# Kernel tuning notes

Hardware: AMD Instinct MI355X
Metric: run time of the kernel (lower is better)

The kernel has to match this reference:

```python
import jax, jax.numpy as jnp
import numpy as np

N_NODES = 50000
N_EDGES = 800000
NFEAT, NHID, NCLASS = 512, 128, 16


def _with_self_loops(edge_idx, n):
    loop = jnp.arange(n, dtype=edge_idx.dtype)
    src = jnp.concatenate([edge_idx[0], loop])  # [E+N]
    dst = jnp.concatenate([edge_idx[1], loop])
    return src, dst


def gcn_conv(x, src, dst, W, b, n):
    # GCNConv with add aggregation, self-loops, symmetric normalization.
    h = x @ W  # [N, out]
    ones = jnp.ones(src.shape[0], dtype=h.dtype)
    deg = jax.ops.segment_sum(ones, dst, num_segments=n)  # in-degree incl. self-loops
    dinv = jnp.where(deg > 0, jax.lax.rsqrt(deg), 0.0)
    norm = dinv[src] * dinv[dst]  # [E+N]
    msg = h[src] * norm[:, None]  # gather + scale
    out = jax.ops.segment_sum(msg, dst, num_segments=n)  # scatter-add
    return out + b


def setup_inputs() -> dict:
    key = jax.random.key(0)
    ks = jax.random.split(key, 8)
    x = jax.random.normal(ks[0], (N_NODES, NFEAT), dtype=jnp.float32)
    edge_idx = jax.random.randint(ks[1], (2, N_EDGES), 0, N_NODES, dtype=jnp.int64)
    s1 = 1.0 / np.sqrt(NFEAT)
    s2 = 1.0 / np.sqrt(NHID)
    W1 = jax.random.uniform(ks[2], (NFEAT, NHID), jnp.float32, -s1, s1)
    b1 = jnp.zeros((NHID,), jnp.float32)
    W2 = jax.random.uniform(ks[3], (NHID, NHID), jnp.float32, -s2, s2)
    b2 = jnp.zeros((NHID,), jnp.float32)
    Wc = jax.random.uniform(ks[4], (NHID, NCLASS), jnp.float32, -s2, s2)
    bc = jax.random.uniform(ks[5], (NCLASS,), jnp.float32, -s2, s2)
    return {"x": x, "edge_idx": edge_idx, "W1": W1, "b1": b1, "W2": W2, "b2": b2, "Wc": Wc, "bc": bc}


def reference(x, edge_idx, W1, b1, W2, b2, Wc, bc):
    n = x.shape[0]
    src, dst = _with_self_loops(edge_idx, n)
    h = gcn_conv(x, src, dst, W1, b1, n)
    h = jax.nn.relu(h)  # dropout is identity in eval mode
    h = gcn_conv(h, src, dst, W2, b2, n)
    h = jax.nn.relu(h)
    logits = h @ Wc + bc
    return jax.nn.log_softmax(logits, axis=1)
```

## Files before the change

### kernel.cpp

```cpp
#include <hip/hip_runtime.h>
#include <math.h>

#define NFEAT 512
#define NHID  128
#define NCLASS 16
#define SCAN_BS 512
#define AGG_BLOCKS 2048

typedef __attribute__((ext_vector_type(8))) short short8;
typedef __attribute__((ext_vector_type(4))) float f32x4;

static __device__ __forceinline__ ushort f2b(float f) {
    union { float f; uint u; } v; v.f = f;
    uint r = v.u + 0x7FFFu + ((v.u >> 16) & 1u);
    return (ushort)(r >> 16);
}
static __device__ __forceinline__ float b2f_lo(uint bits) {
    union { uint u; float f; } v; v.u = bits << 16; return v.f;
}
static __device__ __forceinline__ float b2f_hi(uint bits) {
    union { uint u; float f; } v; v.u = bits & 0xffff0000u; return v.f;
}
static __device__ __forceinline__ float b2f(uint bits) {
    union { uint u; float f; } v; v.u = bits << 16; return v.f;
}


__global__ void k_init_deg(int* __restrict__ deg, int n) {
    int i = blockIdx.x * blockDim.x + threadIdx.x;
    if (i < n) deg[i] = 1;
}

__global__ void k_count(const int* __restrict__ dst, int e, int* __restrict__ deg) {
    int i = blockIdx.x * blockDim.x + threadIdx.x;
    if (i < e) atomicAdd(&deg[dst[i]], 1);
}

__global__ void k_dinv(const int* __restrict__ deg, float* __restrict__ dinv,
                       int* __restrict__ gcnt, int* __restrict__ cursor, int n) {
    int i = blockIdx.x * blockDim.x + threadIdx.x;
    if (i < n) {
        dinv[i] = rsqrtf((float)deg[i]);
        gcnt[i] = (deg[i] + 7) >> 3;
        cursor[i] = 0;
    }
}

__global__ void k_scan1(const int* __restrict__ in, int* __restrict__ offs,
                        int* __restrict__ bsum, int n) {
    __shared__ int s[SCAN_BS];
    int t = threadIdx.x;
    int i = blockIdx.x * SCAN_BS + t;
    int v = (i < n) ? in[i] : 0;
    s[t] = v;
    for (int off = 1; off < SCAN_BS; off <<= 1) {
        __syncthreads();
        int x = (t >= off) ? s[t - off] : 0;
        __syncthreads();
        s[t] += x;
    }
    __syncthreads();
    if (i < n) offs[i] = s[t] - v;
    if (t == SCAN_BS - 1) bsum[blockIdx.x] = s[t];
}

__global__ void k_scan2(int* __restrict__ bsum, int* __restrict__ offs, int nb, int n) {
    if (threadIdx.x == 0 && blockIdx.x == 0) {
        int run = 0;
        for (int b = 0; b < nb; b++) { int x = bsum[b]; bsum[b] = run; run += x; }
        offs[n] = run;
    }
}

__global__ void k_scan3(int* __restrict__ offs, const int* __restrict__ bsum, int n) {
    int i = blockIdx.x * SCAN_BS + threadIdx.x;
    if (i < n) offs[i] += bsum[blockIdx.x];
}

__global__ void k_fill_edges(const int* __restrict__ src, const int* __restrict__ dst, int e,
                             const int* __restrict__ goffs, int* __restrict__ cursor,
                             ushort* __restrict__ colp) {
    int i = blockIdx.x * blockDim.x + threadIdx.x;
    if (i < e) {
        int d = dst[i];
        int p = atomicAdd(&cursor[d], 1);
        colp[(size_t)goffs[d] * 8 + p] = (ushort)src[i];
    }
}

__global__ void k_fill_tail(const int* __restrict__ goffs, const int* __restrict__ deg,
                            ushort* __restrict__ colp, int* __restrict__ gnode,
                            ushort* __restrict__ hs, int n) {
    int i = blockIdx.x * blockDim.x + threadIdx.x;
    if (i < 128) {
        int s = i >> 5, f = i & 31;
        hs[((size_t)s * (n + 1) + n) * 32 + f] = 0;
    }
    if (i < n) {
        int g0 = goffs[i], g1 = goffs[i + 1];
        size_t base = (size_t)g0 * 8;
        int d = deg[i];
        int slots = (g1 - g0) * 8;
        colp[base + d - 1] = (ushort)i;
        for (int p = d; p < slots; p++) colp[base + p] = (ushort)n;
        for (int g = g0; g < g1; g++) gnode[g] = i;
        if (i == 0) {
            int G = goffs[n];
            gnode[G] = -1;
            for (int k = 0; k < 16; k++) colp[(size_t)G * 8 + k] = (ushort)n;
        }
    }
}


__global__ void k_tcast(const float* __restrict__ W, ushort* __restrict__ WT, int K) {
    int idx = blockIdx.x * 256 + threadIdx.x;
    if (idx < K * 128) {
        int k = idx >> 7, c = idx & 127;
        WT[(size_t)c * K + k] = f2b(W[idx]);
    }
}


template<int A_F32>
__global__ __launch_bounds__(256) void k_gemm(const void* __restrict__ Aptr,
                                              const ushort* __restrict__ WT,
                                              const float* __restrict__ rowscale,
                                              ushort* __restrict__ Hs, int M, int K) {
    __shared__ ushort As[128][40];
    __shared__ ushort Bs[128][40];

    const int tid = threadIdx.x;
    const int wid = tid >> 6, lane = tid & 63;
    const int wr = wid >> 1, wc = wid & 1;
    const int lr = lane & 15, lk = (lane >> 4) * 8;
    const int rowbase = blockIdx.x * 128;

    f32x4 acc[4][4];
#pragma unroll
    for (int i = 0; i < 4; i++)
#pragma unroll
        for (int j = 0; j < 4; j++) acc[i][j] = (f32x4)0.f;

    const int sr = tid >> 1;
    const int sh = (tid & 1) * 16;

    for (int k0 = 0; k0 < K; k0 += 32) {
        {
            int gr = rowbase + sr;
            ushort tmp[16];
            if (A_F32) {
                const float* A = (const float*)Aptr;
                if (gr < M) {
                    const float* p = A + (size_t)gr * K + k0 + sh;
#pragma unroll
                    for (int q = 0; q < 4; q++) {
                        float4 v = *(const float4*)(p + q * 4);
                        tmp[q * 4 + 0] = f2b(v.x); tmp[q * 4 + 1] = f2b(v.y);
                        tmp[q * 4 + 2] = f2b(v.z); tmp[q * 4 + 3] = f2b(v.w);
                    }
                } else {
#pragma unroll
                    for (int q = 0; q < 16; q++) tmp[q] = 0;
                }
            } else {
                const ushort* A = (const ushort*)Aptr;
                if (gr < M) {
                    const ushort* p = A + (size_t)gr * K + k0 + sh;
                    *(short8*)&tmp[0] = *(const short8*)(p);
                    *(short8*)&tmp[8] = *(const short8*)(p + 8);
                } else {
#pragma unroll
                    for (int q = 0; q < 16; q++) tmp[q] = 0;
                }
            }
            *(short8*)&As[sr][sh]     = *(short8*)&tmp[0];
            *(short8*)&As[sr][sh + 8] = *(short8*)&tmp[8];
        }
        {
#pragma unroll
            for (int t = 0; t < 2; t++) {
                int c = tid + t * 256;
                int row = c >> 2, q = c & 3;
                short8 v = *(const short8*)(WT + (size_t)row * K + k0 + q * 8);
                *(short8*)&Bs[row][q * 8] = v;
            }
        }
        __syncthreads();

        short8 af[4], bfv[4];
#pragma unroll
        for (int i = 0; i < 4; i++) af[i] = *(const short8*)&As[wr * 64 + i * 16 + lr][lk];
#pragma unroll
        for (int j = 0; j < 4; j++) bfv[j] = *(const short8*)&Bs[wc * 64 + j * 16 + lr][lk];
#pragma unroll
        for (int i = 0; i < 4; i++)
#pragma unroll
            for (int j = 0; j < 4; j++)
                acc[i][j] = __builtin_amdgcn_mfma_f32_16x16x32_bf16(af[i], bfv[j], acc[i][j], 0, 0, 0);
        __syncthreads();
    }

#pragma unroll
    for (int i = 0; i < 4; i++) {
#pragma unroll
        for (int r = 0; r < 4; r++) {
            int row = rowbase + wr * 64 + i * 16 + (lane >> 4) * 4 + r;
            if (row < M) {
                float sc = rowscale[row];
#pragma unroll
                for (int j = 0; j < 4; j++) {
                    int slice = wc * 2 + (j >> 1);
                    int f = (j & 1) * 16 + lr;
                    Hs[((size_t)slice * (M + 1) + row) * 32 + f] = f2b(acc[i][j][r] * sc);
                }
            }
        }
    }
}


__global__ __launch_bounds__(256) void k_aggs(const ushort* __restrict__ hs,
                                              const int* __restrict__ goffs,
                                              const ushort* __restrict__ colp,
                                              const int* __restrict__ gnode,
                                              const float* __restrict__ dinv,
                                              const float* __restrict__ bias,
                                              ushort* __restrict__ outp, int n) {
    const int b = blockIdx.x;
    const int s = (b & 7) >> 1;
    const int wid = threadIdx.x >> 6, lane = threadIdx.x & 63;
    const int e8 = lane >> 3, q = lane & 7;

    const int G = goffs[n];
    const int nranks = gridDim.x;
    const int rank = ((b >> 3) * 2 + (b & 1)) * 4 + wid;
    const int run = (G + nranks - 1) / nranks;
    int gs = rank * run;
    if (gs >= G) return;
    int ge = gs + run; if (ge > G) ge = G;
    if (gs > 0) {
        int pv = gnode[gs - 1];
        while (gs < ge && gnode[gs] == pv) gs++;
        if (gs >= ge) return;
    }

    const ushort* hsl = hs + (size_t)s * (n + 1) * 32;
    const float4 bv = *(const float4*)(bias + s * 32 + q * 4);

    int g = gs;
    const ushort* cp = colp + (size_t)g * 8 + e8;
    const int* gp = gnode + g;
    int v = gp[0];
    uint sc0 = cp[0];
    uint sc1 = cp[8];
    float a0 = 0.f, a1 = 0.f, a2 = 0.f, a3 = 0.f;

    while (true) {
        uint sc2 = cp[16];
        int v_n = gp[1];
        uint2 pk = *(const uint2*)(hsl + (size_t)sc0 * 32 + q * 4);
        a0 += b2f_lo(pk.x); a1 += b2f_hi(pk.x);
        a2 += b2f_lo(pk.y); a3 += b2f_hi(pk.y);

        if (v_n != v) {
            float dv = dinv[v];
            float r0 = a0, r1 = a1, r2 = a2, r3 = a3;
#pragma unroll
            for (int off = 8; off <= 32; off <<= 1) {
                r0 += __shfl_xor(r0, off); r1 += __shfl_xor(r1, off);
                r2 += __shfl_xor(r2, off); r3 += __shfl_xor(r3, off);
            }
            r0 = fmaxf(fmaf(r0, dv, bv.x), 0.f);
            r1 = fmaxf(fmaf(r1, dv, bv.y), 0.f);
            r2 = fmaxf(fmaf(r2, dv, bv.z), 0.f);
            r3 = fmaxf(fmaf(r3, dv, bv.w), 0.f);
            if (lane < 8) {
                uint2 u;
                u.x = (uint)f2b(r0) | ((uint)f2b(r1) << 16);
                u.y = (uint)f2b(r2) | ((uint)f2b(r3) << 16);
                *(uint2*)(outp + (size_t)v * 128 + s * 32 + q * 4) = u;
            }
            if (g + 1 >= ge) break;
            v = v_n;
            a0 = a1 = a2 = a3 = 0.f;
        }
        g++; gp++; cp += 8;
        sc0 = sc1; sc1 = sc2;
    }
}


__global__ __launch_bounds__(256) void k_classify(const ushort* __restrict__ h,
                                                  const float* __restrict__ Wc,
                                                  const float* __restrict__ bc,
                                                  float* __restrict__ out, int n) {
    __shared__ float Ws[128 * 16];
    int tid = threadIdx.x;
#pragma unroll
    for (int t = 0; t < 8; t++) Ws[tid + 256 * t] = Wc[tid + 256 * t];
    __syncthreads();

    int wid = tid >> 6, lane = tid & 63;
    int v = blockIdx.x * 4 + wid;
    if (v >= n) return;

    int j = lane & 15, c = lane >> 4;
    const ushort* hv = h + (size_t)v * 128 + c * 32;
    float acc = 0.f;
#pragma unroll
    for (int t = 0; t < 16; t++) {
        uint pk = *(const uint*)(hv + t * 2);
        acc = fmaf(b2f_lo(pk), Ws[(c * 32 + t * 2 + 0) * 16 + j], acc);
        acc = fmaf(b2f_hi(pk), Ws[(c * 32 + t * 2 + 1) * 16 + j], acc);
    }
    acc += __shfl_xor(acc, 16);
    acc += __shfl_xor(acc, 32);
    acc += bc[j];

    float m = acc;
#pragma unroll
    for (int o = 8; o >= 1; o >>= 1) m = fmaxf(m, __shfl_xor(m, o));
    float sum = expf(acc - m);
#pragma unroll
    for (int o = 8; o >= 1; o >>= 1) sum += __shfl_xor(sum, o);
    if (lane < 16) out[(size_t)v * 16 + j] = acc - m - logf(sum);
}


extern "C" void kernel_launch(void* const* d_in, const int* in_sizes, int n_in,
                              void* d_out, int out_size, void* d_ws, size_t ws_size,
                              hipStream_t stream) {
    const float* x  = (const float*)d_in[0];
    const int* eidx = (const int*)d_in[1];
    const float* W1 = (const float*)d_in[2];
    const float* b1 = (const float*)d_in[3];
    const float* W2 = (const float*)d_in[4];
    const float* b2 = (const float*)d_in[5];
    const float* Wc = (const float*)d_in[6];
    const float* bc = (const float*)d_in[7];
    float* out = (float*)d_out;

    const int N = in_sizes[0] / NFEAT;
    const int E = in_sizes[1] / 2;
    const int* src = eidx;
    const int* dst = eidx + E;

    char* p = (char*)d_ws;
    auto alloc = [&](size_t bytes) { char* r = p; p += (bytes + 255) & ~(size_t)255; return r; };
    int*    deg    = (int*)   alloc((size_t)N * 4);
    float*  dinv   = (float*) alloc((size_t)N * 4);
    int*    gcnt   = (int*)   alloc((size_t)N * 4);
    int*    goffs  = (int*)   alloc((size_t)(N + 1) * 4);
    int*    cursor = (int*)   alloc((size_t)N * 4);
    ushort* colp   = (ushort*)alloc(((size_t)E + 8ull * N + 32) * 2);
    int*    gnode  = (int*)   alloc(((size_t)E / 8 + N + 2) * 4);
    int*    bsum   = (int*)   alloc((size_t)256 * 4);
    ushort* W1T    = (ushort*)alloc((size_t)128 * NFEAT * 2);
    ushort* W2T    = (ushort*)alloc((size_t)128 * NHID * 2);
    ushort* hs     = (ushort*)alloc((size_t)(N + 1) * NHID * 2);
    ushort* g1     = (ushort*)alloc((size_t)N * NHID * 2);
    ushort* g2     = (ushort*)alloc((size_t)N * NHID * 2);

    const int nb = (N + SCAN_BS - 1) / SCAN_BS;

    k_init_deg<<<(N + 255) / 256, 256, 0, stream>>>(deg, N);
    k_count<<<(E + 255) / 256, 256, 0, stream>>>(dst, E, deg);
    k_dinv<<<(N + 255) / 256, 256, 0, stream>>>(deg, dinv, gcnt, cursor, N);
    k_scan1<<<nb, SCAN_BS, 0, stream>>>(gcnt, goffs, bsum, N);
    k_scan2<<<1, 64, 0, stream>>>(bsum, goffs, nb, N);
    k_scan3<<<nb, SCAN_BS, 0, stream>>>(goffs, bsum, N);
    k_fill_edges<<<(E + 255) / 256, 256, 0, stream>>>(src, dst, E, goffs, cursor, colp);
    k_fill_tail<<<(N + 255) / 256, 256, 0, stream>>>(goffs, deg, colp, gnode, hs, N);

    k_tcast<<<(NFEAT * 128 + 255) / 256, 256, 0, stream>>>(W1, W1T, NFEAT);
    k_tcast<<<(NHID * 128 + 255) / 256, 256, 0, stream>>>(W2, W2T, NHID);

    const int gblocks = (N + 127) / 128;
    k_gemm<1><<<gblocks, 256, 0, stream>>>(x, W1T, dinv, hs, N, NFEAT);
    k_aggs<<<AGG_BLOCKS, 256, 0, stream>>>(hs, goffs, colp, gnode, dinv, b1, g1, N);
    k_gemm<0><<<gblocks, 256, 0, stream>>>(g1, W2T, dinv, hs, N, NHID);
    k_aggs<<<AGG_BLOCKS, 256, 0, stream>>>(hs, goffs, colp, gnode, dinv, b2, g2, N);
    k_classify<<<(N + 3) / 4, 256, 0, stream>>>(g2, Wc, bc, out, N);
}
```

Baseline: 276.0 us.

## Pack node-end metadata into 32-bit column words and deepen aggregation prefetch

```diff
diff --git a/kernel.cpp b/kernel.cpp
--- a/kernel.cpp
+++ b/kernel.cpp
@@ -20,9 +20,6 @@
 }
 static __device__ __forceinline__ float b2f_hi(uint bits) {
     union { uint u; float f; } v; v.u = bits & 0xffff0000u; return v.f;
-}
-static __device__ __forceinline__ float b2f(uint bits) {
-    union { uint u; float f; } v; v.u = bits << 16; return v.f;
 }
 
 
@@ -79,18 +76,17 @@
 
 __global__ void k_fill_edges(const int* __restrict__ src, const int* __restrict__ dst, int e,
                              const int* __restrict__ goffs, int* __restrict__ cursor,
-                             ushort* __restrict__ colp) {
+                             uint* __restrict__ colp32) {
     int i = blockIdx.x * blockDim.x + threadIdx.x;
     if (i < e) {
         int d = dst[i];
         int p = atomicAdd(&cursor[d], 1);
-        colp[(size_t)goffs[d] * 8 + p] = (ushort)src[i];
+        colp32[(size_t)goffs[d] * 8 + p] = (uint)src[i];
     }
 }
 
 __global__ void k_fill_tail(const int* __restrict__ goffs, const int* __restrict__ deg,
-                            ushort* __restrict__ colp, int* __restrict__ gnode,
-                            ushort* __restrict__ hs, int n) {
+                            uint* __restrict__ colp32, ushort* __restrict__ hs, int n) {
     int i = blockIdx.x * blockDim.x + threadIdx.x;
     if (i < 128) {
         int s = i >> 5, f = i & 31;
@@ -101,23 +97,46 @@
         size_t base = (size_t)g0 * 8;
         int d = deg[i];
         int slots = (g1 - g0) * 8;
-        colp[base + d - 1] = (ushort)i;
-        for (int p = d; p < slots; p++) colp[base + p] = (ushort)n;
-        for (int g = g0; g < g1; g++) gnode[g] = i;
+        colp32[base + d - 1] = (uint)i;
+        for (int p = d; p < slots; p++) colp32[base + p] = (uint)n;
+        uint meta = (uint)(i + 1) << 16;
+        for (int k = slots - 8; k < slots; k++) colp32[base + k] |= meta;
         if (i == 0) {
             int G = goffs[n];
-            gnode[G] = -1;
-            for (int k = 0; k < 16; k++) colp[(size_t)G * 8 + k] = (ushort)n;
-        }
-    }
-}
-
-
-__global__ void k_tcast(const float* __restrict__ W, ushort* __restrict__ WT, int K) {
+            for (int k = 0; k < 32; k++) colp32[(size_t)G * 8 + k] = (uint)n;
+        }
+    }
+}
+
+__global__ void k_rankstart(const uint* __restrict__ colp32, const int* __restrict__ goffs,
+                            int* __restrict__ rankgs, int n) {
+    int r = blockIdx.x * blockDim.x + threadIdx.x;
+    if (r >= AGG_BLOCKS) return;
+    int G = goffs[n];
+    int run = (G + AGG_BLOCKS - 1) / AGG_BLOCKS;
+    int g = r * run;
+    int ge = g + run; if (ge > G) ge = G;
+    if (g >= G) { rankgs[r] = -1; return; }
+    if (g > 0) {
+        while (g < ge && !(colp32[(size_t)(g - 1) * 8] >> 16)) g++;
+        if (g >= ge) { rankgs[r] = -1; return; }
+    }
+    rankgs[r] = g;
+}
+
+
+__global__ void k_tcast(const float* __restrict__ W1, const float* __restrict__ W2,
+                        ushort* __restrict__ W1T, ushort* __restrict__ W2T) {
     int idx = blockIdx.x * 256 + threadIdx.x;
-    if (idx < K * 128) {
+    if (idx < NFEAT * 128) {
         int k = idx >> 7, c = idx & 127;
-        WT[(size_t)c * K + k] = f2b(W[idx]);
+        W1T[(size_t)c * NFEAT + k] = f2b(W1[idx]);
+    } else {
+        int j = idx - NFEAT * 128;
+        if (j < NHID * 128) {
+            int k = j >> 7, c = j & 127;
+            W2T[(size_t)c * NHID + k] = f2b(W2[j]);
+        }
     }
 }
 
@@ -221,9 +240,9 @@
 
 
 __global__ __launch_bounds__(256) void k_aggs(const ushort* __restrict__ hs,
+                                              const uint* __restrict__ colp32,
+                                              const int* __restrict__ rankgs,
                                               const int* __restrict__ goffs,
-                                              const ushort* __restrict__ colp,
-                                              const int* __restrict__ gnode,
                                               const float* __restrict__ dinv,
                                               const float* __restrict__ bias,
                                               ushort* __restrict__ outp, int n) {
@@ -233,48 +252,44 @@
     const int e8 = lane >> 3, q = lane & 7;
 
     const int G = goffs[n];
-    const int nranks = gridDim.x;
     const int rank = ((b >> 3) * 2 + (b & 1)) * 4 + wid;
-    const int run = (G + nranks - 1) / nranks;
-    int gs = rank * run;
-    if (gs >= G) return;
-    int ge = gs + run; if (ge > G) ge = G;
-    if (gs > 0) {
-        int pv = gnode[gs - 1];
-        while (gs < ge && gnode[gs] == pv) gs++;
-        if (gs >= ge) return;
-    }
+    const int run = (G + AGG_BLOCKS - 1) / AGG_BLOCKS;
+    int gs = rankgs[rank];
+    int ge = (rank + 1) * run; if (ge > G) ge = G;
+    if (gs < 0 || gs >= ge) return;
 
     const ushort* hsl = hs + (size_t)s * (n + 1) * 32;
     const float4 bv = *(const float4*)(bias + s * 32 + q * 4);
 
     int g = gs;
-    const ushort* cp = colp + (size_t)g * 8 + e8;
-    const int* gp = gnode + g;
-    int v = gp[0];
-    uint sc0 = cp[0];
-    uint sc1 = cp[8];
+    const uint* cp = colp32 + (size_t)g * 8 + e8;
+    uint cw0 = cp[0], cw1 = cp[8], cw2 = cp[16];
+    uint2 pk0 = *(const uint2*)(hsl + (size_t)(cw0 & 0xffffu) * 32 + q * 4);
+    uint2 pk1 = *(const uint2*)(hsl + (size_t)(cw1 & 0xffffu) * 32 + q * 4);
+    float fdv0 = (cw0 >> 16) ? dinv[(cw0 >> 16) - 1] : 0.f;
+    float fdv1 = (cw1 >> 16) ? dinv[(cw1 >> 16) - 1] : 0.f;
     float a0 = 0.f, a1 = 0.f, a2 = 0.f, a3 = 0.f;
 
     while (true) {
-        uint sc2 = cp[16];
-        int v_n = gp[1];
-        uint2 pk = *(const uint2*)(hsl + (size_t)sc0 * 32 + q * 4);
-        a0 += b2f_lo(pk.x); a1 += b2f_hi(pk.x);
-        a2 += b2f_lo(pk.y); a3 += b2f_hi(pk.y);
-
-        if (v_n != v) {
-            float dv = dinv[v];
+        uint cw3 = cp[24];
+        uint2 pk2 = *(const uint2*)(hsl + (size_t)(cw2 & 0xffffu) * 32 + q * 4);
+        float fdv2 = (cw2 >> 16) ? dinv[(cw2 >> 16) - 1] : 0.f;
+
+        a0 += b2f_lo(pk0.x); a1 += b2f_hi(pk0.x);
+        a2 += b2f_lo(pk0.y); a3 += b2f_hi(pk0.y);
+
+        if (cw0 >> 16) {
+            int v = (int)(cw0 >> 16) - 1;
             float r0 = a0, r1 = a1, r2 = a2, r3 = a3;
 #pragma unroll
             for (int off = 8; off <= 32; off <<= 1) {
                 r0 += __shfl_xor(r0, off); r1 += __shfl_xor(r1, off);
                 r2 += __shfl_xor(r2, off); r3 += __shfl_xor(r3, off);
             }
-            r0 = fmaxf(fmaf(r0, dv, bv.x), 0.f);
-            r1 = fmaxf(fmaf(r1, dv, bv.y), 0.f);
-            r2 = fmaxf(fmaf(r2, dv, bv.z), 0.f);
-            r3 = fmaxf(fmaf(r3, dv, bv.w), 0.f);
+            r0 = fmaxf(fmaf(r0, fdv0, bv.x), 0.f);
+            r1 = fmaxf(fmaf(r1, fdv0, bv.y), 0.f);
+            r2 = fmaxf(fmaf(r2, fdv0, bv.z), 0.f);
+            r3 = fmaxf(fmaf(r3, fdv0, bv.w), 0.f);
             if (lane < 8) {
                 uint2 u;
                 u.x = (uint)f2b(r0) | ((uint)f2b(r1) << 16);
@@ -282,11 +297,12 @@
                 *(uint2*)(outp + (size_t)v * 128 + s * 32 + q * 4) = u;
             }
             if (g + 1 >= ge) break;
-            v = v_n;
             a0 = a1 = a2 = a3 = 0.f;
         }
-        g++; gp++; cp += 8;
-        sc0 = sc1; sc1 = sc2;
+        g++; cp += 8;
+        cw0 = cw1; cw1 = cw2; cw2 = cw3;
+        pk0 = pk1; pk1 = pk2;
+        fdv0 = fdv1; fdv1 = fdv2;
     }
 }
 
@@ -353,8 +369,8 @@
     int*    gcnt   = (int*)   alloc((size_t)N * 4);
     int*    goffs  = (int*)   alloc((size_t)(N + 1) * 4);
     int*    cursor = (int*)   alloc((size_t)N * 4);
-    ushort* colp   = (ushort*)alloc(((size_t)E + 8ull * N + 32) * 2);
-    int*    gnode  = (int*)   alloc(((size_t)E / 8 + N + 2) * 4);
+    uint*   colp32 = (uint*)  alloc(((size_t)E + 8ull * N + 32) * 4);
+    int*    rankgs = (int*)   alloc((size_t)AGG_BLOCKS * 4);
     int*    bsum   = (int*)   alloc((size_t)256 * 4);
     ushort* W1T    = (ushort*)alloc((size_t)128 * NFEAT * 2);
     ushort* W2T    = (ushort*)alloc((size_t)128 * NHID * 2);
@@ -370,16 +386,16 @@
     k_scan1<<<nb, SCAN_BS, 0, stream>>>(gcnt, goffs, bsum, N);
     k_scan2<<<1, 64, 0, stream>>>(bsum, goffs, nb, N);
     k_scan3<<<nb, SCAN_BS, 0, stream>>>(goffs, bsum, N);
-    k_fill_edges<<<(E + 255) / 256, 256, 0, stream>>>(src, dst, E, goffs, cursor, colp);
-    k_fill_tail<<<(N + 255) / 256, 256, 0, stream>>>(goffs, deg, colp, gnode, hs, N);
-
-    k_tcast<<<(NFEAT * 128 + 255) / 256, 256, 0, stream>>>(W1, W1T, NFEAT);
-    k_tcast<<<(NHID * 128 + 255) / 256, 256, 0, stream>>>(W2, W2T, NHID);
+    k_fill_edges<<<(E + 255) / 256, 256, 0, stream>>>(src, dst, E, goffs, cursor, colp32);
+    k_fill_tail<<<(N + 255) / 256, 256, 0, stream>>>(goffs, deg, colp32, hs, N);
+    k_rankstart<<<(AGG_BLOCKS + 255) / 256, 256, 0, stream>>>(colp32, goffs, rankgs, N);
+
+    k_tcast<<<((NFEAT + NHID) * 128 + 255) / 256, 256, 0, stream>>>(W1, W2, W1T, W2T);
 
     const int gblocks = (N + 127) / 128;
     k_gemm<1><<<gblocks, 256, 0, stream>>>(x, W1T, dinv, hs, N, NFEAT);
-    k_aggs<<<AGG_BLOCKS, 256, 0, stream>>>(hs, goffs, colp, gnode, dinv, b1, g1, N);
+    k_aggs<<<AGG_BLOCKS, 256, 0, stream>>>(hs, colp32, rankgs, goffs, dinv, b1, g1, N);
     k_gemm<0><<<gblocks, 256, 0, stream>>>(g1, W2T, dinv, hs, N, NHID);
-    k_aggs<<<AGG_BLOCKS, 256, 0, stream>>>(hs, goffs, colp, gnode, dinv, b2, g2, N);
+    k_aggs<<<AGG_BLOCKS, 256, 0, stream>>>(hs, colp32, rankgs, goffs, dinv, b2, g2, N);
     k_classify<<<(N + 3) / 4, 256, 0, stream>>>(g2, Wc, bc, out, N);
 }
```

Measured after the change: 266.6 us. 1.04x faster.
